# Kernel tuning notes

Measured on AMD Instinct MI355X. Metric: run time of the kernel, lower is better.

## Reference

```python
import jax, jax.numpy as jnp
import numpy as np

B, N = 16, 48
NODE, EDGE, HID, MSG, LAYERS, TGT = 32, 16, 64, 64, 3, 128
NL = 128  # hidden width of cfg.net_layers / cfg.layers MLPs


def _lin(key, i, o):
    k1, k2 = jax.random.split(key)
    return (jax.random.normal(k1, (i, o), jnp.float32) * 0.05,
            jax.random.normal(k2, (o,), jnp.float32) * 0.05)


def setup_inputs() -> dict:
    key = jax.random.key(0)
    ks = jax.random.split(key, 16)
    g = (jax.random.uniform(ks[0], (B, N, N)) < 0.5).astype(jnp.float32)
    h0 = jax.random.normal(ks[1], (B, N, NODE), jnp.float32)
    e = jax.random.normal(ks[2], (B, N, N, EDGE), jnp.float32)
    msg_w0, msg_b0 = _lin(ks[3], EDGE, NL)
    msg_w1, msg_b1 = _lin(ks[4], NL, NL)
    msg_w2, msg_b2 = _lin(ks[5], NL, MSG * HID)
    gru_wih = jax.random.normal(ks[6], (3 * HID, MSG), jnp.float32) * 0.05
    gru_whh = jax.random.normal(ks[7], (3 * HID, HID), jnp.float32) * 0.05
    gru_bih = jax.random.normal(ks[8], (3 * HID,), jnp.float32) * 0.05
    gru_bhh = jax.random.normal(ks[9], (3 * HID,), jnp.float32) * 0.05
    r0_w0, r0_b0 = _lin(ks[10], 2 * HID, NL)
    r0_w1, r0_b1 = _lin(ks[11], NL, NL)
    r0_w2, r0_b2 = _lin(ks[12], NL, TGT)
    r1_w0, r1_b0 = _lin(ks[13], HID, NL)
    r1_w1, r1_b1 = _lin(ks[14], NL, NL)
    r1_w2, r1_b2 = _lin(ks[15], NL, TGT)
    return dict(g=g, h0=h0, e=e,
                msg_w0=msg_w0, msg_b0=msg_b0, msg_w1=msg_w1, msg_b1=msg_b1,
                msg_w2=msg_w2, msg_b2=msg_b2,
                gru_wih=gru_wih, gru_whh=gru_whh, gru_bih=gru_bih, gru_bhh=gru_bhh,
                r0_w0=r0_w0, r0_b0=r0_b0, r0_w1=r0_w1, r0_b1=r0_b1, r0_w2=r0_w2, r0_b2=r0_b2,
                r1_w0=r1_w0, r1_b0=r1_b0, r1_w1=r1_w1, r1_b1=r1_b1, r1_w2=r1_w2, r1_b2=r1_b2)


def _net(x, w0, b0, w1, b1, w2, b2):
    # Net: relu hidden layers, linear output (matches torch Net with 2 hidden layers)
    x = jax.nn.relu(x @ w0 + b0)
    x = jax.nn.relu(x @ w1 + b1)
    return x @ w2 + b2


def _gru_step(x, h, wih, whh, bih, bhh):
    # torch.nn.GRU single step; gate order r, z, n
    gi = x @ wih.T + bih
    gh = h @ whh.T + bhh
    r = jax.nn.sigmoid(gi[:, :HID] + gh[:, :HID])
    z = jax.nn.sigmoid(gi[:, HID:2 * HID] + gh[:, HID:2 * HID])
    n = jnp.tanh(gi[:, 2 * HID:] + r * gh[:, 2 * HID:])
    return (1.0 - z) * n + z * h


def reference(g, h0, e,
              msg_w0, msg_b0, msg_w1, msg_b1, msg_w2, msg_b2,
              gru_wih, gru_whh, gru_bih, gru_bhh,
              r0_w0, r0_b0, r0_w1, r0_b1, r0_w2, r0_b2,
              r1_w0, r1_b0, r1_w1, r1_b1, r1_w2, r1_b2):
    # pad h0 up to hidden size
    h_first = jnp.concatenate(
        [h0, jnp.zeros((B, N, HID - NODE), h0.dtype)], axis=2)
    node_mask = (jnp.sum(h0, axis=2) > 0).astype(h0.dtype)[..., None]  # [B,N,1]

    # per-edge weight matrices from edge features (same every layer in the
    # original torch code, so compute once): [B*N*N, MSG, HID]
    m_w = _net(e.reshape(-1, EDGE), msg_w0, msg_b0, msg_w1, msg_b1,
               msg_w2, msg_b2).reshape(-1, MSG, HID)

    h_t = h_first
    for _ in range(LAYERS):
        h_feat = h_t.reshape(-1, HID)  # [B*N, HID]
        # faithful to torch: expand on last dim then view(-1, HID),
        # which interleaves the hidden and neighbor axes in memory order
        h_w_rows = jnp.broadcast_to(
            h_feat[:, :, None], (B * N, HID, N)).reshape(-1, HID)
        msg = jnp.einsum('emh,eh->em', m_w, h_w_rows)  # [B*N*N, MSG]
        msg = msg.reshape(B, N, N, MSG)
        agg = jnp.sum(g[..., None] * msg, axis=1)  # masked sum over dim 1 -> [B,N,MSG]
        h_new = _gru_step(agg.reshape(-1, MSG), h_t.reshape(-1, HID),
                          gru_wih, gru_whh, gru_bih, gru_bhh).reshape(B, N, HID)
        h_t = node_mask * h_new

    # readout: Net0(cat[h_0, h_T]) * Net1(h_T), masked by h_0 activity, summed over nodes
    gate_in = jnp.concatenate([h_first, h_t], axis=-1)  # [B,N,2*HID]
    nn_res = (_net(gate_in, r0_w0, r0_b0, r0_w1, r0_b1, r0_w2, r0_b2) *
              _net(h_t, r1_w0, r1_b0, r1_w1, r1_b1, r1_w2, r1_b2))  # [B,N,TGT]
    read_mask = (jnp.sum(h_first, axis=2) > 0).astype(nn_res.dtype)[..., None]
    res = jnp.sum(read_mask * nn_res, axis=1)  # [B,TGT]
    return jax.nn.sigmoid(res)
```

## Files before the change

### kernel.cpp

```cpp
#include <hip/hip_runtime.h>
#include <cmath>

#define B_ 16
#define N_ 48
#define HID_ 64
#define NL_ 128
#define NNODE_ (B_*N_)
#define NEDGE_ (B_*N_*N_)

__device__ __forceinline__ float sigmoidf_(float x){ return 1.0f/(1.0f+expf(-x)); }

__global__ void k_prep(const float* __restrict__ w2, const float* __restrict__ b2,
                       const float* __restrict__ h0,
                       const float* __restrict__ wih, const float* __restrict__ whh,
                       const float* __restrict__ w1,
                       float* __restrict__ A, float* __restrict__ Bm,
                       float* __restrict__ Ab, float* __restrict__ Bb,
                       float* __restrict__ hfirst, float* __restrict__ mask,
                       float* __restrict__ wihT, float* __restrict__ whhT,
                       float* __restrict__ w1T)
{
    int idx = blockIdx.x*256 + threadIdx.x;
    if (idx < 24576) {
        int r = idx >> 13;
        int c = (idx >> 6) & 127;
        int m = idx & 63;
        int t = 48 - 16*r;
        const float* src = w2 + c*4096 + m*64;
        float a = 0.f, b = 0.f;
        for (int k = 0; k < 64; k++){ float v = src[k]; if (k < t) a += v; else b += v; }
        A[idx] = a; Bm[idx] = b;
    } else if (idx < 24768) {
        int i2 = idx - 24576;
        int r = i2 >> 6, m = i2 & 63;
        int t = 48 - 16*r;
        const float* src = b2 + m*64;
        float a = 0.f, b = 0.f;
        for (int k = 0; k < 64; k++){ float v = src[k]; if (k < t) a += v; else b += v; }
        Ab[i2] = a; Bb[i2] = b;
    } else if (idx < 73920) {
        int i3 = idx - 24768;
        int node = i3 >> 6, m = i3 & 63;
        hfirst[i3] = (m < 32) ? h0[node*32 + m] : 0.f;
        if (m == 0) {
            float s = 0.f;
            for (int k = 0; k < 32; k++) s += h0[node*32 + k];
            mask[node] = (s > 0.f) ? 1.f : 0.f;
        }
    } else if (idx < 98496) {
        int i4 = idx - 73920;
        if (i4 < 12288) {
            int k = i4 / 192, col = i4 - k*192;
            wihT[i4] = wih[col*64 + k];
        } else {
            int i5 = i4 - 12288;
            int k = i5 / 192, col = i5 - k*192;
            whhT[i5] = whh[col*64 + k];
        }
    } else if (idx < 114880) {
        int i6 = idx - 98496;
        int o = i6 >> 7, i = i6 & 127;
        w1T[i6] = w1[i*128 + o];
    }
}

__global__ __launch_bounds__(256) void k_mlp(
    const float* __restrict__ ein, const float* __restrict__ w0, const float* __restrict__ b0,
    const float* __restrict__ w1T, const float* __restrict__ b1,
    float* __restrict__ relu2)
{
    __shared__ __align__(16) float x1s[64*132];
    int tid = threadIdx.x;
    int et = tid & 15, ot = tid >> 4;
    int o0 = ot * 8;
    size_t e0 = (size_t)blockIdx.x * 64;

    float acc[4][8];
    {
        float4 ba = *(const float4*)&b0[o0];
        float4 bb = *(const float4*)&b0[o0 + 4];
        #pragma unroll
        for (int q = 0; q < 4; q++){
            acc[q][0]=ba.x; acc[q][1]=ba.y; acc[q][2]=ba.z; acc[q][3]=ba.w;
            acc[q][4]=bb.x; acc[q][5]=bb.y; acc[q][6]=bb.z; acc[q][7]=bb.w;
        }
    }
    #pragma unroll
    for (int i4 = 0; i4 < 4; i4++){
        float4 ev[4];
        #pragma unroll
        for (int q = 0; q < 4; q++)
            ev[q] = *(const float4*)&ein[(e0 + q*16 + et)*16 + i4*4];
        #pragma unroll
        for (int d = 0; d < 4; d++){
            int i = i4*4 + d;
            float4 wa = *(const float4*)&w0[i*128 + o0];
            float4 wb = *(const float4*)&w0[i*128 + o0 + 4];
            #pragma unroll
            for (int q = 0; q < 4; q++){
                float xi = (d==0) ? ev[q].x : (d==1) ? ev[q].y : (d==2) ? ev[q].z : ev[q].w;
                acc[q][0] += xi*wa.x; acc[q][1] += xi*wa.y;
                acc[q][2] += xi*wa.z; acc[q][3] += xi*wa.w;
                acc[q][4] += xi*wb.x; acc[q][5] += xi*wb.y;
                acc[q][6] += xi*wb.z; acc[q][7] += xi*wb.w;
            }
        }
    }
    #pragma unroll
    for (int q = 0; q < 4; q++){
        int e = q*16 + et;
        float4 s0 = make_float4(fmaxf(acc[q][0],0.f), fmaxf(acc[q][1],0.f),
                                fmaxf(acc[q][2],0.f), fmaxf(acc[q][3],0.f));
        float4 s1 = make_float4(fmaxf(acc[q][4],0.f), fmaxf(acc[q][5],0.f),
                                fmaxf(acc[q][6],0.f), fmaxf(acc[q][7],0.f));
        *(float4*)&x1s[e*132 + o0]     = s0;
        *(float4*)&x1s[e*132 + o0 + 4] = s1;
    }
    __syncthreads();

    float a2[4][8];
    {
        float4 ba = *(const float4*)&b1[o0];
        float4 bb = *(const float4*)&b1[o0 + 4];
        #pragma unroll
        for (int q = 0; q < 4; q++){
            a2[q][0]=ba.x; a2[q][1]=ba.y; a2[q][2]=ba.z; a2[q][3]=ba.w;
            a2[q][4]=bb.x; a2[q][5]=bb.y; a2[q][6]=bb.z; a2[q][7]=bb.w;
        }
    }
    for (int i4 = 0; i4 < 32; i4++){
        int i = i4*4;
        float4 wv[8];
        #pragma unroll
        for (int r2 = 0; r2 < 8; r2++)
            wv[r2] = *(const float4*)&w1T[(size_t)(o0 + r2)*128 + i];
        #pragma unroll
        for (int q = 0; q < 4; q++){
            float4 xv = *(const float4*)&x1s[(q*16 + et)*132 + i];
            #pragma unroll
            for (int r2 = 0; r2 < 8; r2++){
                a2[q][r2] += xv.x*wv[r2].x + xv.y*wv[r2].y
                           + xv.z*wv[r2].z + xv.w*wv[r2].w;
            }
        }
    }
    #pragma unroll
    for (int q = 0; q < 4; q++){
        size_t e = e0 + q*16 + et;
        float4 s0 = make_float4(fmaxf(a2[q][0],0.f), fmaxf(a2[q][1],0.f),
                                fmaxf(a2[q][2],0.f), fmaxf(a2[q][3],0.f));
        float4 s1 = make_float4(fmaxf(a2[q][4],0.f), fmaxf(a2[q][5],0.f),
                                fmaxf(a2[q][6],0.f), fmaxf(a2[q][7],0.f));
        *(float4*)&relu2[e*128 + o0]     = s0;
        *(float4*)&relu2[e*128 + o0 + 4] = s1;
    }
}

__global__ __launch_bounds__(256) void k_layer(
    const float* __restrict__ hin, float* __restrict__ hout,
    const float* __restrict__ relu2,
    const float* __restrict__ A, const float* __restrict__ Bm,
    const float* __restrict__ Ab, const float* __restrict__ Bb,
    const float* __restrict__ g, const float* __restrict__ mask,
    const float* __restrict__ wihT, const float* __restrict__ whhT,
    const float* __restrict__ bih, const float* __restrict__ bhh)
{
    int bj = blockIdx.x;
    int b = bj / 48, j = bj - b*48;
    int r = j % 3;
    int p0 = j + j/3;
    int tid = threadIdx.x;
    int base = b*48;
    __shared__ float hs[64], wAs[48], wBs[48];
    __shared__ float pU[2][128], pV[2][128];
    __shared__ float Us[128], Vs[128];
    __shared__ float pC[4][64];
    __shared__ float sAB[2];
    __shared__ float aggs[64], gi[192], gh[192];

    if (tid < 64) hs[tid] = hin[(size_t)bj*64 + tid];
    else if (tid < 112){
        int i = tid - 64;
        int node = base + i;
        float gv = g[(size_t)node*48 + j];
        wAs[i] = gv * hin[(size_t)node*64 + p0];
        wBs[i] = gv * hin[(size_t)node*64 + p0 + 1];
    }
    __syncthreads();
    if (tid < 2){
        const float* src = tid ? wBs : wAs;
        float s = 0.f;
        for (int i = 0; i < 48; i++) s += src[i];
        sAB[tid] = s;
    }
    {
        int c = tid & 127, half = tid >> 7;
        const float* r2b = relu2 + ((size_t)base*48 + j)*128 + c;
        float aU = 0.f, aV = 0.f;
        for (int ii = 0; ii < 24; ii++){
            int i = half*24 + ii;
            float v = r2b[(size_t)i*6144];
            aU += wAs[i]*v; aV += wBs[i]*v;
        }
        pU[half][c] = aU; pV[half][c] = aV;
    }
    __syncthreads();
    if (tid < 128){ Us[tid] = pU[0][tid] + pU[1][tid]; Vs[tid] = pV[0][tid] + pV[1][tid]; }
    __syncthreads();
    {
        int m = tid & 63, cg = tid >> 6;
        const float* Arp = A  + r*8192 + m;
        const float* Brp = Bm + r*8192 + m;
        float a = 0.f;
        for (int cc = 0; cc < 32; cc++){
            int c = cg*32 + cc;
            a += Us[c]*Arp[c*64] + Vs[c]*Brp[c*64];
        }
        pC[cg][m] = a;
    }
    __syncthreads();
    if (tid < 64){
        aggs[tid] = pC[0][tid] + pC[1][tid] + pC[2][tid] + pC[3][tid]
                  + sAB[0]*Ab[r*64 + tid] + sAB[1]*Bb[r*64 + tid];
    }
    __syncthreads();
    if (tid < 192){
        float gacc = bih[tid], hacc = bhh[tid];
        for (int k = 0; k < 64; k++){
            gacc += aggs[k] * wihT[k*192 + tid];
            hacc += hs[k]   * whhT[k*192 + tid];
        }
        gi[tid] = gacc; gh[tid] = hacc;
    }
    __syncthreads();
    if (tid < 64){
        float rr = sigmoidf_(gi[tid] + gh[tid]);
        float zz = sigmoidf_(gi[64+tid] + gh[64+tid]);
        float nn = tanhf(gi[128+tid] + rr*gh[128+tid]);
        float hnew = (1.f - zz)*nn + zz*hs[tid];
        hout[(size_t)bj*64 + tid] = mask[bj] * hnew;
    }
}

__device__ __forceinline__ void rd_layer(
    const float* __restrict__ Xs, const float* __restrict__ W,
    const float* __restrict__ bias, float* __restrict__ Ys,
    int dim, int o, int ng, bool do_relu)
{
    float a0 = bias[o];
    float a1 = a0;
    for (int i = 0; i < dim; i += 4){
        float w0 = W[(size_t)(i+0)*128 + o];
        float w1 = W[(size_t)(i+1)*128 + o];
        float w2 = W[(size_t)(i+2)*128 + o];
        float w3 = W[(size_t)(i+3)*128 + o];
        const float4 x0 = *(const float4*)&Xs[ng*128 + i];
        const float4 x1 = *(const float4*)&Xs[(ng+2)*128 + i];
        a0 += x0.x*w0 + x0.y*w1 + x0.z*w2 + x0.w*w3;
        a1 += x1.x*w0 + x1.y*w1 + x1.z*w2 + x1.w*w3;
    }
    if (do_relu){ a0 = fmaxf(a0, 0.f); a1 = fmaxf(a1, 0.f); }
    Ys[ng*128 + o] = a0;
    Ys[(ng+2)*128 + o] = a1;
}

__global__ __launch_bounds__(256) void k_read(
    const float* __restrict__ hfirst, const float* __restrict__ hT,
    const float* __restrict__ mask,
    const float* __restrict__ w00, const float* __restrict__ b00,
    const float* __restrict__ w01, const float* __restrict__ b01,
    const float* __restrict__ w02, const float* __restrict__ b02,
    const float* __restrict__ w10, const float* __restrict__ b10,
    const float* __restrict__ w11, const float* __restrict__ b11,
    const float* __restrict__ w12, const float* __restrict__ b12,
    float* __restrict__ partial)
{
    __shared__ __align__(16) float xs[4*128];
    __shared__ __align__(16) float ys[4*128];
    __shared__ __align__(16) float zs[4*128];
    __shared__ __align__(16) float os0[4*128];
    __shared__ float mS[4];
    int tid = threadIdx.x;
    int b = blockIdx.x / 12, gg = blockIdx.x - b*12;
    int node0 = b*48 + gg*4;
    int o = tid & 127, ng = tid >> 7;
    if (tid < 4) mS[tid] = mask[node0 + tid];
    for (int i = tid; i < 4*128; i += 256){
        int r = i >> 7, c = i & 127;
        xs[i] = (c < 64) ? hfirst[(size_t)(node0+r)*64 + c]
                         : hT[(size_t)(node0+r)*64 + (c - 64)];
    }
    __syncthreads();
    rd_layer(xs,      w00, b00, ys,  128, o, ng, true);  __syncthreads();
    rd_layer(ys,      w01, b01, zs,  128, o, ng, true);  __syncthreads();
    rd_layer(zs,      w02, b02, os0, 128, o, ng, false); __syncthreads();
    rd_layer(xs + 64, w10, b10, ys,  64,  o, ng, true);  __syncthreads();
    rd_layer(ys,      w11, b11, zs,  128, o, ng, true);  __syncthreads();
    {
        float a0 = b12[o];
        float a1 = a0;
        for (int i = 0; i < 128; i += 4){
            float w0 = w12[(size_t)(i+0)*128 + o];
            float w1 = w12[(size_t)(i+1)*128 + o];
            float w2 = w12[(size_t)(i+2)*128 + o];
            float w3 = w12[(size_t)(i+3)*128 + o];
            const float4 x0 = *(const float4*)&zs[ng*128 + i];
            const float4 x1 = *(const float4*)&zs[(ng+2)*128 + i];
            a0 += x0.x*w0 + x0.y*w1 + x0.z*w2 + x0.w*w3;
            a1 += x1.x*w0 + x1.y*w1 + x1.z*w2 + x1.w*w3;
        }
        float s = mS[ng]   * os0[ng*128 + o]     * a0
                + mS[ng+2] * os0[(ng+2)*128 + o] * a1;
        __syncthreads();
        ys[ng*128 + o] = s;
    }
    __syncthreads();
    if (tid < 128)
        partial[(size_t)blockIdx.x*128 + tid] = ys[tid] + ys[128 + tid];
}

__global__ void k_final(const float* __restrict__ partial, float* __restrict__ out)
{
    int idx = blockIdx.x*256 + threadIdx.x;
    if (idx < B_*128){
        int b = idx >> 7, t = idx & 127;
        float s = 0.f;
        for (int c = 0; c < 12; c++) s += partial[(size_t)(b*12 + c)*128 + t];
        out[idx] = 1.0f / (1.0f + expf(-s));
    }
}

extern "C" void kernel_launch(void* const* d_in, const int* in_sizes, int n_in,
                              void* d_out, int out_size, void* d_ws, size_t ws_size,
                              hipStream_t stream)
{
    (void)in_sizes; (void)n_in; (void)out_size; (void)ws_size;
    const float* g    = (const float*)d_in[0];
    const float* h0   = (const float*)d_in[1];
    const float* e    = (const float*)d_in[2];
    const float* mw0  = (const float*)d_in[3];
    const float* mb0  = (const float*)d_in[4];
    const float* mw1  = (const float*)d_in[5];
    const float* mb1  = (const float*)d_in[6];
    const float* mw2  = (const float*)d_in[7];
    const float* mb2  = (const float*)d_in[8];
    const float* wih  = (const float*)d_in[9];
    const float* whh  = (const float*)d_in[10];
    const float* bih  = (const float*)d_in[11];
    const float* bhh  = (const float*)d_in[12];
    const float* r0w0 = (const float*)d_in[13];
    const float* r0b0 = (const float*)d_in[14];
    const float* r0w1 = (const float*)d_in[15];
    const float* r0b1 = (const float*)d_in[16];
    const float* r0w2 = (const float*)d_in[17];
    const float* r0b2 = (const float*)d_in[18];
    const float* r1w0 = (const float*)d_in[19];
    const float* r1b0 = (const float*)d_in[20];
    const float* r1w1 = (const float*)d_in[21];
    const float* r1b1 = (const float*)d_in[22];
    const float* r1w2 = (const float*)d_in[23];
    const float* r1b2 = (const float*)d_in[24];
    float* out = (float*)d_out;

    float* ws     = (float*)d_ws;
    float* A      = ws;
    float* Bm     = A      + 24576;
    float* Ab     = Bm     + 24576;
    float* Bb     = Ab     + 192;
    float* hfirst = Bb     + 192;
    float* hA     = hfirst + 49152;
    float* hB     = hA     + 49152;
    float* mask   = hB     + 49152;
    float* wihT   = mask   + 768;
    float* whhT   = wihT   + 12288;
    float* w1T    = whhT   + 12288;
    float* part   = w1T    + 16384;
    float* relu2  = part   + 24576;

    k_prep<<<449, 256, 0, stream>>>(mw2, mb2, h0, wih, whh, mw1,
                                    A, Bm, Ab, Bb, hfirst, mask, wihT, whhT, w1T);
    k_mlp<<<576, 256, 0, stream>>>(e, mw0, mb0, w1T, mb1, relu2);
    k_layer<<<768, 256, 0, stream>>>(hfirst, hA, relu2, A, Bm, Ab, Bb, g, mask,
                                     wihT, whhT, bih, bhh);
    k_layer<<<768, 256, 0, stream>>>(hA, hB, relu2, A, Bm, Ab, Bb, g, mask,
                                     wihT, whhT, bih, bhh);
    k_layer<<<768, 256, 0, stream>>>(hB, hA, relu2, A, Bm, Ab, Bb, g, mask,
                                     wihT, whhT, bih, bhh);
    k_read<<<192, 256, 0, stream>>>(hfirst, hA, mask,
                                    r0w0, r0b0, r0w1, r0b1, r0w2, r0b2,
                                    r1w0, r1b0, r1w1, r1b1, r1w2, r1b2, part);
    k_final<<<8, 256, 0, stream>>>(part, out);
}
```

Baseline: 192.8 us.

## Fuse prep into MLP kernel, transpose relu2 layout, fold final reduction via atomics

Merges the weight-prep kernel into the edge-MLP kernel as extra blocks and drops the w1 transpose by reading w1 row-major directly. It halves edges per block to 32 for more blocks, and stores relu2 transposed so each layer block reads a contiguous 48x128 slab instead of strided rows. The final sigmoid kernel is removed: readout blocks atomically accumulate and the last arriving block per batch applies the sigmoid. This trades kernel-launch overhead and strided reads for atomics and a non-deterministic summation order.

New measurement: 223.0 us. 1.16x slower.

```diff
diff --git a/kernel.cpp b/kernel.cpp
--- a/kernel.cpp
+++ b/kernel.cpp
@@ -3,93 +3,90 @@
 
 #define B_ 16
 #define N_ 48
-#define HID_ 64
-#define NL_ 128
-#define NNODE_ (B_*N_)
-#define NEDGE_ (B_*N_*N_)
 
 __device__ __forceinline__ float sigmoidf_(float x){ return 1.0f/(1.0f+expf(-x)); }
 
-__global__ void k_prep(const float* __restrict__ w2, const float* __restrict__ b2,
-                       const float* __restrict__ h0,
-                       const float* __restrict__ wih, const float* __restrict__ whh,
-                       const float* __restrict__ w1,
-                       float* __restrict__ A, float* __restrict__ Bm,
-                       float* __restrict__ Ab, float* __restrict__ Bb,
-                       float* __restrict__ hfirst, float* __restrict__ mask,
-                       float* __restrict__ wihT, float* __restrict__ whhT,
-                       float* __restrict__ w1T)
+__global__ __launch_bounds__(256) void k_mlp_prep(
+    const float* __restrict__ ein, const float* __restrict__ w0, const float* __restrict__ b0,
+    const float* __restrict__ w1, const float* __restrict__ b1,
+    const float* __restrict__ w2, const float* __restrict__ b2,
+    const float* __restrict__ h0,
+    const float* __restrict__ wih, const float* __restrict__ whh,
+    float* __restrict__ relu2T,
+    float* __restrict__ A, float* __restrict__ Bm,
+    float* __restrict__ Ab, float* __restrict__ Bb,
+    float* __restrict__ hfirst, float* __restrict__ mask,
+    float* __restrict__ wihT, float* __restrict__ whhT,
+    float* __restrict__ accum, unsigned* __restrict__ cnt)
 {
-    int idx = blockIdx.x*256 + threadIdx.x;
-    if (idx < 24576) {
-        int r = idx >> 13;
-        int c = (idx >> 6) & 127;
-        int m = idx & 63;
-        int t = 48 - 16*r;
-        const float* src = w2 + c*4096 + m*64;
-        float a = 0.f, b = 0.f;
-        for (int k = 0; k < 64; k++){ float v = src[k]; if (k < t) a += v; else b += v; }
-        A[idx] = a; Bm[idx] = b;
-    } else if (idx < 24768) {
-        int i2 = idx - 24576;
-        int r = i2 >> 6, m = i2 & 63;
-        int t = 48 - 16*r;
-        const float* src = b2 + m*64;
-        float a = 0.f, b = 0.f;
-        for (int k = 0; k < 64; k++){ float v = src[k]; if (k < t) a += v; else b += v; }
-        Ab[i2] = a; Bb[i2] = b;
-    } else if (idx < 73920) {
-        int i3 = idx - 24768;
-        int node = i3 >> 6, m = i3 & 63;
-        hfirst[i3] = (m < 32) ? h0[node*32 + m] : 0.f;
-        if (m == 0) {
-            float s = 0.f;
-            for (int k = 0; k < 32; k++) s += h0[node*32 + k];
-            mask[node] = (s > 0.f) ? 1.f : 0.f;
-        }
-    } else if (idx < 98496) {
-        int i4 = idx - 73920;
-        if (i4 < 12288) {
-            int k = i4 / 192, col = i4 - k*192;
-            wihT[i4] = wih[col*64 + k];
-        } else {
-            int i5 = i4 - 12288;
-            int k = i5 / 192, col = i5 - k*192;
-            whhT[i5] = whh[col*64 + k];
-        }
-    } else if (idx < 114880) {
-        int i6 = idx - 98496;
-        int o = i6 >> 7, i = i6 & 127;
-        w1T[i6] = w1[i*128 + o];
-    }
-}
-
-__global__ __launch_bounds__(256) void k_mlp(
-    const float* __restrict__ ein, const float* __restrict__ w0, const float* __restrict__ b0,
-    const float* __restrict__ w1T, const float* __restrict__ b1,
-    float* __restrict__ relu2)
-{
-    __shared__ __align__(16) float x1s[64*132];
+    __shared__ __align__(16) float x1s[32*132];
+
+    if (blockIdx.x >= 1152){
+        int idx = (blockIdx.x - 1152)*256 + threadIdx.x;
+        if (idx < 24576) {
+            int r = idx >> 13;
+            int c = (idx >> 6) & 127;
+            int m = idx & 63;
+            int t = 48 - 16*r;
+            const float* src = w2 + c*4096 + m*64;
+            float a = 0.f, b = 0.f;
+            for (int k = 0; k < 64; k++){ float v = src[k]; if (k < t) a += v; else b += v; }
+            A[idx] = a; Bm[idx] = b;
+        } else if (idx < 24768) {
+            int i2 = idx - 24576;
+            int r = i2 >> 6, m = i2 & 63;
+            int t = 48 - 16*r;
+            const float* src = b2 + m*64;
+            float a = 0.f, b = 0.f;
+            for (int k = 0; k < 64; k++){ float v = src[k]; if (k < t) a += v; else b += v; }
+            Ab[i2] = a; Bb[i2] = b;
+        } else if (idx < 73920) {
+            int i3 = idx - 24768;
+            int node = i3 >> 6, m = i3 & 63;
+            hfirst[i3] = (m < 32) ? h0[node*32 + m] : 0.f;
+            if (m == 0) {
+                float s = 0.f;
+                for (int k = 0; k < 32; k++) s += h0[node*32 + k];
+                mask[node] = (s > 0.f) ? 1.f : 0.f;
+            }
+        } else if (idx < 98496) {
+            int i4 = idx - 73920;
+            if (i4 < 12288) {
+                int k = i4 / 192, col = i4 - k*192;
+                wihT[i4] = wih[col*64 + k];
+            } else {
+                int i5 = i4 - 12288;
+                int k = i5 / 192, col = i5 - k*192;
+                whhT[i5] = whh[col*64 + k];
+            }
+        } else if (idx < 100544) {
+            int i6 = idx - 98496;
+            accum[i6] = 0.f;
+        } else if (idx < 100560) {
+            cnt[idx - 100544] = 0u;
+        }
+        return;
+    }
+
     int tid = threadIdx.x;
-    int et = tid & 15, ot = tid >> 4;
-    int o0 = ot * 8;
-    size_t e0 = (size_t)blockIdx.x * 64;
-
-    float acc[4][8];
+    int et = tid & 15, o0 = (tid >> 4) * 8;
+    size_t e0 = (size_t)blockIdx.x * 32;
+
+    float acc[2][8];
     {
         float4 ba = *(const float4*)&b0[o0];
         float4 bb = *(const float4*)&b0[o0 + 4];
         #pragma unroll
-        for (int q = 0; q < 4; q++){
+        for (int q = 0; q < 2; q++){
             acc[q][0]=ba.x; acc[q][1]=ba.y; acc[q][2]=ba.z; acc[q][3]=ba.w;
             acc[q][4]=bb.x; acc[q][5]=bb.y; acc[q][6]=bb.z; acc[q][7]=bb.w;
         }
     }
     #pragma unroll
     for (int i4 = 0; i4 < 4; i4++){
-        float4 ev[4];
-        #pragma unroll
-        for (int q = 0; q < 4; q++)
+        float4 ev[2];
+        #pragma unroll
+        for (int q = 0; q < 2; q++)
             ev[q] = *(const float4*)&ein[(e0 + q*16 + et)*16 + i4*4];
         #pragma unroll
         for (int d = 0; d < 4; d++){
@@ -97,7 +94,7 @@
             float4 wa = *(const float4*)&w0[i*128 + o0];
             float4 wb = *(const float4*)&w0[i*128 + o0 + 4];
             #pragma unroll
-            for (int q = 0; q < 4; q++){
+            for (int q = 0; q < 2; q++){
                 float xi = (d==0) ? ev[q].x : (d==1) ? ev[q].y : (d==2) ? ev[q].z : ev[q].w;
                 acc[q][0] += xi*wa.x; acc[q][1] += xi*wa.y;
                 acc[q][2] += xi*wa.z; acc[q][3] += xi*wa.w;
@@ -107,58 +104,74 @@
         }
     }
     #pragma unroll
-    for (int q = 0; q < 4; q++){
-        int e = q*16 + et;
-        float4 s0 = make_float4(fmaxf(acc[q][0],0.f), fmaxf(acc[q][1],0.f),
-                                fmaxf(acc[q][2],0.f), fmaxf(acc[q][3],0.f));
-        float4 s1 = make_float4(fmaxf(acc[q][4],0.f), fmaxf(acc[q][5],0.f),
-                                fmaxf(acc[q][6],0.f), fmaxf(acc[q][7],0.f));
-        *(float4*)&x1s[e*132 + o0]     = s0;
-        *(float4*)&x1s[e*132 + o0 + 4] = s1;
-    }
-    __syncthreads();
-
-    float a2[4][8];
+    for (int q = 0; q < 2; q++){
+        int el = q*16 + et;
+        *(float4*)&x1s[el*132 + o0] =
+            make_float4(fmaxf(acc[q][0],0.f), fmaxf(acc[q][1],0.f),
+                        fmaxf(acc[q][2],0.f), fmaxf(acc[q][3],0.f));
+        *(float4*)&x1s[el*132 + o0 + 4] =
+            make_float4(fmaxf(acc[q][4],0.f), fmaxf(acc[q][5],0.f),
+                        fmaxf(acc[q][6],0.f), fmaxf(acc[q][7],0.f));
+    }
+    __syncthreads();
+
+    float a2[2][8];
     {
         float4 ba = *(const float4*)&b1[o0];
         float4 bb = *(const float4*)&b1[o0 + 4];
         #pragma unroll
-        for (int q = 0; q < 4; q++){
+        for (int q = 0; q < 2; q++){
             a2[q][0]=ba.x; a2[q][1]=ba.y; a2[q][2]=ba.z; a2[q][3]=ba.w;
             a2[q][4]=bb.x; a2[q][5]=bb.y; a2[q][6]=bb.z; a2[q][7]=bb.w;
         }
     }
     for (int i4 = 0; i4 < 32; i4++){
         int i = i4*4;
-        float4 wv[8];
-        #pragma unroll
-        for (int r2 = 0; r2 < 8; r2++)
-            wv[r2] = *(const float4*)&w1T[(size_t)(o0 + r2)*128 + i];
-        #pragma unroll
-        for (int q = 0; q < 4; q++){
-            float4 xv = *(const float4*)&x1s[(q*16 + et)*132 + i];
-            #pragma unroll
-            for (int r2 = 0; r2 < 8; r2++){
-                a2[q][r2] += xv.x*wv[r2].x + xv.y*wv[r2].y
-                           + xv.z*wv[r2].z + xv.w*wv[r2].w;
-            }
+        float4 w0a = *(const float4*)&w1[(size_t)(i+0)*128 + o0];
+        float4 w0b = *(const float4*)&w1[(size_t)(i+0)*128 + o0 + 4];
+        float4 w1a = *(const float4*)&w1[(size_t)(i+1)*128 + o0];
+        float4 w1b = *(const float4*)&w1[(size_t)(i+1)*128 + o0 + 4];
+        float4 w2a = *(const float4*)&w1[(size_t)(i+2)*128 + o0];
+        float4 w2b = *(const float4*)&w1[(size_t)(i+2)*128 + o0 + 4];
+        float4 w3a = *(const float4*)&w1[(size_t)(i+3)*128 + o0];
+        float4 w3b = *(const float4*)&w1[(size_t)(i+3)*128 + o0 + 4];
+        float4 xv[2];
+        #pragma unroll
+        for (int q = 0; q < 2; q++)
+            xv[q] = *(const float4*)&x1s[(q*16 + et)*132 + i];
+        #pragma unroll
+        for (int q = 0; q < 2; q++){
+            float4 x = xv[q];
+            a2[q][0] += x.x*w0a.x + x.y*w1a.x + x.z*w2a.x + x.w*w3a.x;
+            a2[q][1] += x.x*w0a.y + x.y*w1a.y + x.z*w2a.y + x.w*w3a.y;
+            a2[q][2] += x.x*w0a.z + x.y*w1a.z + x.z*w2a.z + x.w*w3a.z;
+            a2[q][3] += x.x*w0a.w + x.y*w1a.w + x.z*w2a.w + x.w*w3a.w;
+            a2[q][4] += x.x*w0b.x + x.y*w1b.x + x.z*w2b.x + x.w*w3b.x;
+            a2[q][5] += x.x*w0b.y + x.y*w1b.y + x.z*w2b.y + x.w*w3b.y;
+            a2[q][6] += x.x*w0b.z + x.y*w1b.z + x.z*w2b.z + x.w*w3b.z;
+            a2[q][7] += x.x*w0b.w + x.y*w1b.w + x.z*w2b.w + x.w*w3b.w;
         }
     }
     #pragma unroll
-    for (int q = 0; q < 4; q++){
+    for (int q = 0; q < 2; q++){
         size_t e = e0 + q*16 + et;
+        int b  = (int)(e / 2304);
+        int rm = (int)(e - (size_t)b*2304);
+        int i  = rm / 48;
+        int j  = rm - i*48;
+        size_t off = (((size_t)(b*48 + j)*48) + i)*128;
         float4 s0 = make_float4(fmaxf(a2[q][0],0.f), fmaxf(a2[q][1],0.f),
                                 fmaxf(a2[q][2],0.f), fmaxf(a2[q][3],0.f));
         float4 s1 = make_float4(fmaxf(a2[q][4],0.f), fmaxf(a2[q][5],0.f),
                                 fmaxf(a2[q][6],0.f), fmaxf(a2[q][7],0.f));
-        *(float4*)&relu2[e*128 + o0]     = s0;
-        *(float4*)&relu2[e*128 + o0 + 4] = s1;
+        *(float4*)&relu2T[off + o0]     = s0;
+        *(float4*)&relu2T[off + o0 + 4] = s1;
     }
 }
 
 __global__ __launch_bounds__(256) void k_layer(
     const float* __restrict__ hin, float* __restrict__ hout,
-    const float* __restrict__ relu2,
+    const float* __restrict__ relu2T,
     const float* __restrict__ A, const float* __restrict__ Bm,
     const float* __restrict__ Ab, const float* __restrict__ Bb,
     const float* __restrict__ g, const float* __restrict__ mask,
@@ -195,11 +208,11 @@
     }
     {
         int c = tid & 127, half = tid >> 7;
-        const float* r2b = relu2 + ((size_t)base*48 + j)*128 + c;
+        const float* r2b = relu2T + (size_t)bj*6144 + c;
         float aU = 0.f, aV = 0.f;
         for (int ii = 0; ii < 24; ii++){
             int i = half*24 + ii;
-            float v = r2b[(size_t)i*6144];
+            float v = r2b[i*128];
             aU += wAs[i]*v; aV += wBs[i]*v;
         }
         pU[half][c] = aU; pV[half][c] = aV;
@@ -264,7 +277,7 @@
     Ys[(ng+2)*128 + o] = a1;
 }
 
-__global__ __launch_bounds__(256) void k_read(
+__global__ __launch_bounds__(256) void k_read_final(
     const float* __restrict__ hfirst, const float* __restrict__ hT,
     const float* __restrict__ mask,
     const float* __restrict__ w00, const float* __restrict__ b00,
@@ -273,13 +286,15 @@
     const float* __restrict__ w10, const float* __restrict__ b10,
     const float* __restrict__ w11, const float* __restrict__ b11,
     const float* __restrict__ w12, const float* __restrict__ b12,
-    float* __restrict__ partial)
+    float* __restrict__ accum, unsigned* __restrict__ cnt,
+    float* __restrict__ out)
 {
     __shared__ __align__(16) float xs[4*128];
     __shared__ __align__(16) float ys[4*128];
     __shared__ __align__(16) float zs[4*128];
     __shared__ __align__(16) float os0[4*128];
     __shared__ float mS[4];
+    __shared__ unsigned fin;
     int tid = threadIdx.x;
     int b = blockIdx.x / 12, gg = blockIdx.x - b*12;
     int node0 = b*48 + gg*4;
@@ -316,17 +331,16 @@
     }
     __syncthreads();
     if (tid < 128)
-        partial[(size_t)blockIdx.x*128 + tid] = ys[tid] + ys[128 + tid];
-}
-
-__global__ void k_final(const float* __restrict__ partial, float* __restrict__ out)
-{
-    int idx = blockIdx.x*256 + threadIdx.x;
-    if (idx < B_*128){
-        int b = idx >> 7, t = idx & 127;
-        float s = 0.f;
-        for (int c = 0; c < 12; c++) s += partial[(size_t)(b*12 + c)*128 + t];
-        out[idx] = 1.0f / (1.0f + expf(-s));
+        atomicAdd(&accum[(size_t)b*128 + tid], ys[tid] + ys[128 + tid]);
+    __syncthreads();
+    if (tid == 0){
+        __threadfence();
+        fin = atomicAdd(&cnt[b], 1u);
+    }
+    __syncthreads();
+    if (fin == 11u && tid < 128){
+        float v = atomicAdd(&accum[(size_t)b*128 + tid], 0.f);
+        out[(size_t)b*128 + tid] = 1.0f / (1.0f + expf(-v));
     }
 }
 
@@ -373,21 +387,22 @@
     float* mask   = hB     + 49152;
     float* wihT   = mask   + 768;
     float* whhT   = wihT   + 12288;
-    float* w1T    = whhT   + 12288;
-    float* part   = w1T    + 16384;
-    float* relu2  = part   + 24576;
-
-    k_prep<<<449, 256, 0, stream>>>(mw2, mb2, h0, wih, whh, mw1,
-                                    A, Bm, Ab, Bb, hfirst, mask, wihT, whhT, w1T);
-    k_mlp<<<576, 256, 0, stream>>>(e, mw0, mb0, w1T, mb1, relu2);
-    k_layer<<<768, 256, 0, stream>>>(hfirst, hA, relu2, A, Bm, Ab, Bb, g, mask,
+    float* accum  = whhT   + 12288;
+    unsigned* cnt = (unsigned*)(accum + 2048);
+    float* relu2T = accum  + 2048 + 64;
+
+    k_mlp_prep<<<1545, 256, 0, stream>>>(e, mw0, mb0, mw1, mb1, mw2, mb2, h0,
+                                         wih, whh, relu2T,
+                                         A, Bm, Ab, Bb, hfirst, mask,
+                                         wihT, whhT, accum, cnt);
+    k_layer<<<768, 256, 0, stream>>>(hfirst, hA, relu2T, A, Bm, Ab, Bb, g, mask,
                                      wihT, whhT, bih, bhh);
-    k_layer<<<768, 256, 0, stream>>>(hA, hB, relu2, A, Bm, Ab, Bb, g, mask,
+    k_layer<<<768, 256, 0, stream>>>(hA, hB, relu2T, A, Bm, Ab, Bb, g, mask,
                                      wihT, whhT, bih, bhh);
-    k_layer<<<768, 256, 0, stream>>>(hB, hA, relu2, A, Bm, Ab, Bb, g, mask,
+    k_layer<<<768, 256, 0, stream>>>(hB, hA, relu2T, A, Bm, Ab, Bb, g, mask,
                                      wihT, whhT, bih, bhh);
-    k_read<<<192, 256, 0, stream>>>(hfirst, hA, mask,
-                                    r0w0, r0b0, r0w1, r0b1, r0w2, r0b2,
-                                    r1w0, r1b0, r1w1, r1b1, r1w2, r1b2, part);
-    k_final<<<8, 256, 0, stream>>>(part, out);
+    k_read_final<<<192, 256, 0, stream>>>(hfirst, hA, mask,
+                                          r0w0, r0b0, r0w1, r0b1, r0w2, r0b2,
+                                          r1w0, r1b0, r1w1, r1b1, r1w2, r1b2,
+                                          accum, cnt, out);
 }
```
